# Performance work log

Measured on AMD Instinct MI355X. Metric: run time of the kernel, lower is better.

Reference implementation:

```python
import jax, jax.numpy as jnp
import numpy as np

# PointPillars PillarFeatureNet defaults
VX, VY, VZ = 0.2, 0.2, 4.0
X_OFF = VX / 2 + 0.0
Y_OFF = VY / 2 + (-40.0)
Z_OFF = VZ / 2 + (-3.0)
BN_EPS = 1e-3
N, M, C_RAW, C_IN, C_OUT = 100000, 32, 4, 10, 64


def setup_inputs() -> dict:
    key = jax.random.key(0)
    k1, k2, k3, k4, k5, k6 = jax.random.split(key, 6)
    features = jax.random.normal(k1, (N, M, C_RAW), dtype=jnp.float32)
    num_points = jax.random.randint(k2, (N,), 1, M + 1, dtype=jnp.int32)
    coors = jax.random.randint(k3, (N, 4), 0, 400, dtype=jnp.int32)
    # PFNLayer params: Linear(10 -> 64, bias=False) + BatchNorm1d(64) (eval stats)
    W = jax.random.normal(k4, (C_OUT, C_IN), dtype=jnp.float32) * (1.0 / np.sqrt(C_IN))
    gamma = jnp.ones((C_OUT,), jnp.float32)
    beta = jnp.zeros((C_OUT,), jnp.float32)
    running_mean = jax.random.normal(k5, (C_OUT,), dtype=jnp.float32) * 0.1
    running_var = jnp.abs(jax.random.normal(k6, (C_OUT,), dtype=jnp.float32)) * 0.1 + 0.9
    return {"features": features, "num_points": num_points, "coors": coors,
            "W": W, "gamma": gamma, "beta": beta,
            "running_mean": running_mean, "running_var": running_var}


def reference(features, num_points, coors, W, gamma, beta, running_mean, running_var):
    np_f = num_points.astype(features.dtype)[:, None, None]            # (N,1,1)
    xyz = features[:, :, :3]                                           # (N,M,3)
    # cluster center offset
    points_mean = jnp.sum(xyz, axis=1, keepdims=True) / np_f           # (N,1,3)
    f_cluster = xyz - points_mean                                      # (N,M,3)
    # voxel center offset (coors layout: [batch, z, y, x])
    cz = coors[:, 0].astype(features.dtype)[:, None]
    cy = coors[:, 1].astype(features.dtype)[:, None]
    cx = coors[:, 2].astype(features.dtype)[:, None]
    f_center = jnp.stack([
        features[:, :, 0] - (cx * VX + X_OFF),
        features[:, :, 1] - (cy * VY + Y_OFF),
        features[:, :, 2] - (cz * VZ + Z_OFF),
    ], axis=-1)                                                        # (N,M,3)
    feats = jnp.concatenate([features, f_cluster, f_center], axis=-1)  # (N,M,10)
    # padding mask
    mask = (jnp.arange(M, dtype=jnp.int32)[None, :] < num_points[:, None])
    feats = feats * mask[:, :, None].astype(feats.dtype)
    # PFNLayer: Linear -> BN(eval) -> GELU -> max over points
    x = jnp.einsum('nmc,oc->nmo', feats, W)                            # (N,M,64)
    inv_std = jax.lax.rsqrt(running_var + BN_EPS)
    x = (x - running_mean) * (inv_std * gamma) + beta
    x = jax.nn.gelu(x, approximate=False)
    return jnp.max(x, axis=1)                                          # (N,64)
```

## Files before the change

### kernel.cpp

```cpp
#include <hip/hip_runtime.h>
#include <cmath>


__device__ __forceinline__ float gelu_exact(float x) {
    return 0.5f * x * (1.0f + erff(x * 0.70710678118654752440f));
}

__global__ __launch_bounds__(256) void pfn_kernel(
    const float* __restrict__ features,
    const int*   __restrict__ num_points,
    const int*   __restrict__ coors,
    const float* __restrict__ W,
    const float* __restrict__ gamma,
    const float* __restrict__ beta,
    const float* __restrict__ rmean,
    const float* __restrict__ rvar,
    float*       __restrict__ out,
    int nTotal)
{
    __shared__ float4 lds[4][64];

    const int lane = threadIdx.x & 63;
    const int wid  = threadIdx.x >> 6;
    const int waveGlobal = blockIdx.x * 4 + wid;
    const int waveCount  = gridDim.x * 4;
    const int nPairs = (nTotal + 1) >> 1;

    const int o = lane;
    const float w0 = W[o*10+0], w1 = W[o*10+1], w2 = W[o*10+2], w3 = W[o*10+3],
                w4 = W[o*10+4], w5 = W[o*10+5], w6 = W[o*10+6], w7 = W[o*10+7],
                w8 = W[o*10+8], w9 = W[o*10+9];
    const float a = gamma[o] / sqrtf(rvar[o] + 1e-3f);
    const float b = fmaf(-rmean[o], a, beta[o]);
    const float A0 = a*(w0+w4+w7), A1 = a*(w1+w5+w8), A2 = a*(w2+w6+w9), A3 = a*w3;

    for (int p = waveGlobal; p < nPairs; p += waveCount) {
        const int iA = 2*p;
        const int iB = (2*p + 1 < nTotal) ? (2*p + 1) : (nTotal - 1);
        const bool hasB = (2*p + 1 < nTotal);

        const float4* fb = reinterpret_cast<const float4*>(features) + (size_t)p * 64;
        float4 f = fb[lane];
        lds[wid][lane] = f;

        float sx = f.x, sy = f.y, sz = f.z;
        #pragma unroll
        for (int d = 1; d < 32; d <<= 1) {
            sx += __shfl_xor(sx, d);
            sy += __shfl_xor(sy, d);
            sz += __shfl_xor(sz, d);
        }
        const float tx = __shfl_xor(sx, 32), ty = __shfl_xor(sy, 32), tz = __shfl_xor(sz, 32);
        const bool lo = (lane < 32);
        const float sAx = lo ? sx : tx, sAy = lo ? sy : ty, sAz = lo ? sz : tz;
        const float sBx = lo ? tx : sx, sBy = lo ? ty : sy, sBz = lo ? tz : sz;

        const int nA = num_points[iA];
        const int nB = num_points[iB];
        const int4 cA = reinterpret_cast<const int4*>(coors)[iA];
        const int4 cB = reinterpret_cast<const int4*>(coors)[iB];

        const float mAx = sAx / (float)nA, mAy = sAy / (float)nA, mAz = sAz / (float)nA;
        const float mBx = sBx / (float)nB, mBy = sBy / (float)nB, mBz = sBz / (float)nB;

        const float ccxA = fmaf((float)cA.z, 0.2f,   0.1f);
        const float ccyA = fmaf((float)cA.y, 0.2f, -39.9f);
        const float cczA = fmaf((float)cA.x, 4.0f,  -1.0f);
        const float ccxB = fmaf((float)cB.z, 0.2f,   0.1f);
        const float ccyB = fmaf((float)cB.y, 0.2f, -39.9f);
        const float cczB = fmaf((float)cB.x, 4.0f,  -1.0f);

        const float KA = -(mAx*w4 + mAy*w5 + mAz*w6 + ccxA*w7 + ccyA*w8 + cczA*w9);
        const float KB = -(mBx*w4 + mBy*w5 + mBz*w6 + ccxB*w7 + ccyB*w8 + cczB*w9);
        const float CA = fmaf(a, KA, b);
        const float CB = fmaf(a, KB, b);

        __asm__ volatile("s_waitcnt lgkmcnt(0)" ::: "memory");

        float vmaxA = -INFINITY, vminA = INFINITY;
        const float4* la = &lds[wid][0];
        for (int m = 0; m < nA; ++m) {
            float4 t = la[m];
            float y = fmaf(t.x, A0, fmaf(t.y, A1, fmaf(t.z, A2, fmaf(t.w, A3, CA))));
            vmaxA = fmaxf(vmaxA, y);
            vminA = fminf(vminA, y);
        }
        float vmaxB = -INFINITY, vminB = INFINITY;
        const float4* lb = &lds[wid][32];
        for (int m = 0; m < nB; ++m) {
            float4 t = lb[m];
            float y = fmaf(t.x, A0, fmaf(t.y, A1, fmaf(t.z, A2, fmaf(t.w, A3, CB))));
            vmaxB = fmaxf(vmaxB, y);
            vminB = fminf(vminB, y);
        }
        if (nA < 32) { vmaxA = fmaxf(vmaxA, b); vminA = fminf(vminA, b); }
        if (nB < 32) { vmaxB = fmaxf(vmaxB, b); vminB = fminf(vminB, b); }

        const float rA = fmaxf(gelu_exact(vmaxA), gelu_exact(vminA));
        const float rB = fmaxf(gelu_exact(vmaxB), gelu_exact(vminB));

        out[(size_t)iA * 64 + o] = rA;
        if (hasB) out[(size_t)iB * 64 + o] = rB;
    }
}

extern "C" void kernel_launch(void* const* d_in, const int* in_sizes, int n_in,
                              void* d_out, int out_size, void* d_ws, size_t ws_size,
                              hipStream_t stream) {
    const float* features   = (const float*)d_in[0];
    const int*   num_points = (const int*)  d_in[1];
    const int*   coors      = (const int*)  d_in[2];
    const float* W          = (const float*)d_in[3];
    const float* gamma      = (const float*)d_in[4];
    const float* beta       = (const float*)d_in[5];
    const float* rmean      = (const float*)d_in[6];
    const float* rvar       = (const float*)d_in[7];
    float* out = (float*)d_out;

    const int nTotal = in_sizes[1];

    pfn_kernel<<<2048, 256, 0, stream>>>(features, num_points, coors, W,
                                         gamma, beta, rmean, rvar, out, nTotal);
}
```

Baseline: 135.3 us.

## Transpose pillar points to SoA in LDS and process 8 points per iteration with packed FMA

Stores each pillar's points in structure-of-arrays form in LDS, padding invalid slots with a copy of point 0 so that points can be processed in chunks of 8 without a tail. The inner min/max loop uses v2f packed FMAs with four independent accumulators to raise ILP and allow packed-math issue. Division by the point count is replaced with a hardware reciprocal. The risk is extra shuffles and LDS writes per pair, plus up to 7 wasted points per pillar.

```diff
diff --git a/kernel.cpp b/kernel.cpp
--- a/kernel.cpp
+++ b/kernel.cpp
@@ -2,8 +2,47 @@
 #include <cmath>
 
 
+typedef float v2f __attribute__((ext_vector_type(2)));
+
 __device__ __forceinline__ float gelu_exact(float x) {
     return 0.5f * x * (1.0f + erff(x * 0.70710678118654752440f));
+}
+
+__device__ __forceinline__ void pillar_minmax(const float* __restrict__ R, int n,
+                                              v2f a0, v2f a1, v2f a2, v2f a3, v2f cc,
+                                              float& oMax, float& oMin)
+{
+    float vmx0 = -INFINITY, vmx1 = -INFINITY, vmx2 = -INFINITY, vmx3 = -INFINITY;
+    float vmn0 =  INFINITY, vmn1 =  INFINITY, vmn2 =  INFINITY, vmn3 =  INFINITY;
+    const int t = (n + 7) >> 3;
+    for (int c = 0; c < t; ++c) {
+        const float4* px = (const float4*)(R +   0 + c * 8);
+        const float4* py = (const float4*)(R +  32 + c * 8);
+        const float4* pz = (const float4*)(R +  64 + c * 8);
+        const float4* pw = (const float4*)(R +  96 + c * 8);
+        float4 xa = px[0], xb = px[1];
+        float4 ya = py[0], yb = py[1];
+        float4 za = pz[0], zb = pz[1];
+        float4 wa = pw[0], wb = pw[1];
+        v2f X0 = {xa.x, xa.y}, X1 = {xa.z, xa.w}, X2 = {xb.x, xb.y}, X3 = {xb.z, xb.w};
+        v2f Y0 = {ya.x, ya.y}, Y1 = {ya.z, ya.w}, Y2 = {yb.x, yb.y}, Y3 = {yb.z, yb.w};
+        v2f Z0 = {za.x, za.y}, Z1 = {za.z, za.w}, Z2 = {zb.x, zb.y}, Z3 = {zb.z, zb.w};
+        v2f W0 = {wa.x, wa.y}, W1 = {wa.z, wa.w}, W2 = {wb.x, wb.y}, W3 = {wb.z, wb.w};
+        v2f y0 = __builtin_elementwise_fma(X0, a0, __builtin_elementwise_fma(Y0, a1,
+                 __builtin_elementwise_fma(Z0, a2, __builtin_elementwise_fma(W0, a3, cc))));
+        v2f y1 = __builtin_elementwise_fma(X1, a0, __builtin_elementwise_fma(Y1, a1,
+                 __builtin_elementwise_fma(Z1, a2, __builtin_elementwise_fma(W1, a3, cc))));
+        v2f y2 = __builtin_elementwise_fma(X2, a0, __builtin_elementwise_fma(Y2, a1,
+                 __builtin_elementwise_fma(Z2, a2, __builtin_elementwise_fma(W2, a3, cc))));
+        v2f y3 = __builtin_elementwise_fma(X3, a0, __builtin_elementwise_fma(Y3, a1,
+                 __builtin_elementwise_fma(Z3, a2, __builtin_elementwise_fma(W3, a3, cc))));
+        vmx0 = fmaxf(fmaxf(y0.x, y0.y), vmx0);  vmn0 = fminf(fminf(y0.x, y0.y), vmn0);
+        vmx1 = fmaxf(fmaxf(y1.x, y1.y), vmx1);  vmn1 = fminf(fminf(y1.x, y1.y), vmn1);
+        vmx2 = fmaxf(fmaxf(y2.x, y2.y), vmx2);  vmn2 = fminf(fminf(y2.x, y2.y), vmn2);
+        vmx3 = fmaxf(fmaxf(y3.x, y3.y), vmx3);  vmn3 = fminf(fminf(y3.x, y3.y), vmn3);
+    }
+    oMax = fmaxf(fmaxf(vmx0, vmx1), fmaxf(vmx2, vmx3));
+    oMin = fminf(fminf(vmn0, vmn1), fminf(vmn2, vmn3));
 }
 
 __global__ __launch_bounds__(256) void pfn_kernel(
@@ -18,13 +57,14 @@
     float*       __restrict__ out,
     int nTotal)
 {
-    __shared__ float4 lds[4][64];
+    __shared__ float lds[4][2 * 4 * 32];
 
     const int lane = threadIdx.x & 63;
     const int wid  = threadIdx.x >> 6;
     const int waveGlobal = blockIdx.x * 4 + wid;
     const int waveCount  = gridDim.x * 4;
     const int nPairs = (nTotal + 1) >> 1;
+    float* slot = &lds[wid][0];
 
     const int o = lane;
     const float w0 = W[o*10+0], w1 = W[o*10+1], w2 = W[o*10+2], w3 = W[o*10+3],
@@ -32,16 +72,16 @@
                 w8 = W[o*10+8], w9 = W[o*10+9];
     const float a = gamma[o] / sqrtf(rvar[o] + 1e-3f);
     const float b = fmaf(-rmean[o], a, beta[o]);
-    const float A0 = a*(w0+w4+w7), A1 = a*(w1+w5+w8), A2 = a*(w2+w6+w9), A3 = a*w3;
+    const float A0s = a*(w0+w4+w7), A1s = a*(w1+w5+w8), A2s = a*(w2+w6+w9), A3s = a*w3;
+    const v2f a0 = {A0s, A0s}, a1 = {A1s, A1s}, a2 = {A2s, A2s}, a3 = {A3s, A3s};
 
     for (int p = waveGlobal; p < nPairs; p += waveCount) {
-        const int iA = 2*p;
-        const int iB = (2*p + 1 < nTotal) ? (2*p + 1) : (nTotal - 1);
-        const bool hasB = (2*p + 1 < nTotal);
+        const int iA = 2 * p;
+        const bool hasB = (2 * p + 1 < nTotal);
+        const int iB = hasB ? (2 * p + 1) : (nTotal - 1);
 
         const float4* fb = reinterpret_cast<const float4*>(features) + (size_t)p * 64;
-        float4 f = fb[lane];
-        lds[wid][lane] = f;
+        const float4 f = fb[lane];
 
         float sx = f.x, sy = f.y, sz = f.z;
         #pragma unroll
@@ -51,17 +91,32 @@
             sz += __shfl_xor(sz, d);
         }
         const float tx = __shfl_xor(sx, 32), ty = __shfl_xor(sy, 32), tz = __shfl_xor(sz, 32);
-        const bool lo = (lane < 32);
-        const float sAx = lo ? sx : tx, sAy = lo ? sy : ty, sAz = lo ? sz : tz;
-        const float sBx = lo ? tx : sx, sBy = lo ? ty : sy, sBz = lo ? tz : sz;
 
         const int nA = num_points[iA];
         const int nB = num_points[iB];
         const int4 cA = reinterpret_cast<const int4*>(coors)[iA];
         const int4 cB = reinterpret_cast<const int4*>(coors)[iB];
 
-        const float mAx = sAx / (float)nA, mAy = sAy / (float)nA, mAz = sAz / (float)nA;
-        const float mBx = sBx / (float)nB, mBy = sBy / (float)nB, mBz = sBz / (float)nB;
+        const int m = lane & 31;
+        const int nOwn = (lane < 32) ? nA : nB;
+        const int src = lane & 32;
+        const float f0x = __shfl(f.x, src), f0y = __shfl(f.y, src),
+                    f0z = __shfl(f.z, src), f0w = __shfl(f.w, src);
+        const bool valid = m < nOwn;
+        const int rbase = (lane >> 5) * 128 + m;
+        slot[rbase +  0] = valid ? f.x : f0x;
+        slot[rbase + 32] = valid ? f.y : f0y;
+        slot[rbase + 64] = valid ? f.z : f0z;
+        slot[rbase + 96] = valid ? f.w : f0w;
+
+        const bool lo = (lane < 32);
+        const float sAx = lo ? sx : tx, sAy = lo ? sy : ty, sAz = lo ? sz : tz;
+        const float sBx = lo ? tx : sx, sBy = lo ? ty : sy, sBz = lo ? tz : sz;
+
+        const float rcA = __builtin_amdgcn_rcpf((float)nA);
+        const float rcB = __builtin_amdgcn_rcpf((float)nB);
+        const float mAx = sAx * rcA, mAy = sAy * rcA, mAz = sAz * rcA;
+        const float mBx = sBx * rcB, mBy = sBy * rcB, mBz = sBz * rcB;
 
         const float ccxA = fmaf((float)cA.z, 0.2f,   0.1f);
         const float ccyA = fmaf((float)cA.y, 0.2f, -39.9f);
@@ -77,22 +132,10 @@
 
         __asm__ volatile("s_waitcnt lgkmcnt(0)" ::: "memory");
 
-        float vmaxA = -INFINITY, vminA = INFINITY;
-        const float4* la = &lds[wid][0];
-        for (int m = 0; m < nA; ++m) {
-            float4 t = la[m];
-            float y = fmaf(t.x, A0, fmaf(t.y, A1, fmaf(t.z, A2, fmaf(t.w, A3, CA))));
-            vmaxA = fmaxf(vmaxA, y);
-            vminA = fminf(vminA, y);
-        }
-        float vmaxB = -INFINITY, vminB = INFINITY;
-        const float4* lb = &lds[wid][32];
-        for (int m = 0; m < nB; ++m) {
-            float4 t = lb[m];
-            float y = fmaf(t.x, A0, fmaf(t.y, A1, fmaf(t.z, A2, fmaf(t.w, A3, CB))));
-            vmaxB = fmaxf(vmaxB, y);
-            vminB = fminf(vminB, y);
-        }
+        float vmaxA, vminA, vmaxB, vminB;
+        pillar_minmax(slot,       nA, a0, a1, a2, a3, (v2f){CA, CA}, vmaxA, vminA);
+        pillar_minmax(slot + 128, nB, a0, a1, a2, a3, (v2f){CB, CB}, vmaxB, vminB);
+
         if (nA < 32) { vmaxA = fmaxf(vmaxA, b); vminA = fminf(vminA, b); }
         if (nB < 32) { vmaxB = fmaxf(vmaxB, b); vminB = fminf(vminB, b); }
 
```

New measurement: 137.4 us. No clear change (+1.6%).

## Load pillar points via scalar loads, one pillar per wave, drop LDS

Applied to the files above, without the earlier changes.

Each wave now handles one pillar and pulls its 32 points, num_points and coors straight into scalar registers with inline-asm s_load_dwordx16 in four chunks. The LDS staging and shuffle reduction are gone. The xyz sums are computed from the scalar values, padded slots are replaced by the first point, and C is added after the max/min reduction. This is meant to remove LDS traffic, shuffle latency and the data-dependent loop, but it serializes each chunk behind an lgkmcnt wait and puts all of the feature bandwidth through the scalar cache.

```diff
diff --git a/kernel.cpp b/kernel.cpp
--- a/kernel.cpp
+++ b/kernel.cpp
@@ -2,8 +2,54 @@
 #include <cmath>
 
 
+typedef float v16f __attribute__((ext_vector_type(16)));
+typedef int   v4i  __attribute__((ext_vector_type(4)));
+
 __device__ __forceinline__ float gelu_exact(float x) {
     return 0.5f * x * (1.0f + erff(x * 0.70710678118654752440f));
+}
+
+__device__ __forceinline__ float dotp(float x, float y, float z, float w,
+                                      float A0, float A1, float A2, float A3) {
+    return fmaf(x, A0, fmaf(y, A1, fmaf(z, A2, w * A3)));
+}
+
+struct Acc { float sx, sy, sz, mx, mn; };
+
+__device__ __forceinline__ void proc_chunk(const v16f u0, const v16f u1, int base, int ns,
+                                           float x0, float y0, float z0, float w0,
+                                           float A0, float A1, float A2, float A3, Acc& ac)
+{
+    ac.sx += ((u0[0] + u0[4]) + (u0[8] + u0[12])) + ((u1[0] + u1[4]) + (u1[8] + u1[12]));
+    ac.sy += ((u0[1] + u0[5]) + (u0[9] + u0[13])) + ((u1[1] + u1[5]) + (u1[9] + u1[13]));
+    ac.sz += ((u0[2] + u0[6]) + (u0[10] + u0[14])) + ((u1[2] + u1[6]) + (u1[10] + u1[14]));
+
+    if (ns >= base + 8) {
+        float p0 = dotp(u0[0],  u0[1],  u0[2],  u0[3],  A0, A1, A2, A3);
+        float p1 = dotp(u0[4],  u0[5],  u0[6],  u0[7],  A0, A1, A2, A3);
+        float p2 = dotp(u0[8],  u0[9],  u0[10], u0[11], A0, A1, A2, A3);
+        float p3 = dotp(u0[12], u0[13], u0[14], u0[15], A0, A1, A2, A3);
+        float p4 = dotp(u1[0],  u1[1],  u1[2],  u1[3],  A0, A1, A2, A3);
+        float p5 = dotp(u1[4],  u1[5],  u1[6],  u1[7],  A0, A1, A2, A3);
+        float p6 = dotp(u1[8],  u1[9],  u1[10], u1[11], A0, A1, A2, A3);
+        float p7 = dotp(u1[12], u1[13], u1[14], u1[15], A0, A1, A2, A3);
+        ac.mx = fmaxf(fmaxf(p6, p7), fmaxf(fmaxf(p4, p5),
+                fmaxf(fmaxf(p2, p3), fmaxf(fmaxf(p0, p1), ac.mx))));
+        ac.mn = fminf(fminf(p6, p7), fminf(fminf(p4, p5),
+                fminf(fminf(p2, p3), fminf(fminf(p0, p1), ac.mn))));
+    } else if (ns > base) {
+        #define DOTSEL(u, j)                                                     \
+            { bool vld = (base + (j)) < ns;                                      \
+              float xs_ = vld ? u[4*(j)+0] : x0;                                 \
+              float ys_ = vld ? u[4*(j)+1] : y0;                                 \
+              float zs_ = vld ? u[4*(j)+2] : z0;                                 \
+              float ws_ = vld ? u[4*(j)+3] : w0;                                 \
+              float pv  = dotp(xs_, ys_, zs_, ws_, A0, A1, A2, A3);              \
+              ac.mx = fmaxf(ac.mx, pv); ac.mn = fminf(ac.mn, pv); }
+        DOTSEL(u0, 0) DOTSEL(u0, 1) DOTSEL(u0, 2) DOTSEL(u0, 3)
+        DOTSEL(u1, 0) DOTSEL(u1, 1) DOTSEL(u1, 2) DOTSEL(u1, 3)
+        #undef DOTSEL
+    }
 }
 
 __global__ __launch_bounds__(256) void pfn_kernel(
@@ -18,15 +64,11 @@
     float*       __restrict__ out,
     int nTotal)
 {
-    __shared__ float4 lds[4][64];
-
-    const int lane = threadIdx.x & 63;
-    const int wid  = threadIdx.x >> 6;
+    const int wid = __builtin_amdgcn_readfirstlane(threadIdx.x) >> 6;
     const int waveGlobal = blockIdx.x * 4 + wid;
     const int waveCount  = gridDim.x * 4;
-    const int nPairs = (nTotal + 1) >> 1;
 
-    const int o = lane;
+    const int o = threadIdx.x & 63;
     const float w0 = W[o*10+0], w1 = W[o*10+1], w2 = W[o*10+2], w3 = W[o*10+3],
                 w4 = W[o*10+4], w5 = W[o*10+5], w6 = W[o*10+6], w7 = W[o*10+7],
                 w8 = W[o*10+8], w9 = W[o*10+9];
@@ -34,73 +76,59 @@
     const float b = fmaf(-rmean[o], a, beta[o]);
     const float A0 = a*(w0+w4+w7), A1 = a*(w1+w5+w8), A2 = a*(w2+w6+w9), A3 = a*w3;
 
-    for (int p = waveGlobal; p < nPairs; p += waveCount) {
-        const int iA = 2*p;
-        const int iB = (2*p + 1 < nTotal) ? (2*p + 1) : (nTotal - 1);
-        const bool hasB = (2*p + 1 < nTotal);
+    for (int i = waveGlobal; i < nTotal; i += waveCount) {
+        const float* fptr = features + (size_t)i * 128;
 
-        const float4* fb = reinterpret_cast<const float4*>(features) + (size_t)p * 64;
-        float4 f = fb[lane];
-        lds[wid][lane] = f;
+        int ns; v4i cr; v16f u0, u1;
+        asm volatile(
+            "s_load_dword %0, %4, 0x0\n\t"
+            "s_load_dwordx4 %1, %5, 0x0\n\t"
+            "s_load_dwordx16 %2, %6, 0x0\n\t"
+            "s_load_dwordx16 %3, %6, 0x40\n\t"
+            "s_waitcnt lgkmcnt(0)"
+            : "=&s"(ns), "=&s"(cr), "=&s"(u0), "=&s"(u1)
+            : "s"(num_points + i), "s"(coors + (size_t)4 * i), "s"(fptr));
 
-        float sx = f.x, sy = f.y, sz = f.z;
-        #pragma unroll
-        for (int d = 1; d < 32; d <<= 1) {
-            sx += __shfl_xor(sx, d);
-            sy += __shfl_xor(sy, d);
-            sz += __shfl_xor(sz, d);
-        }
-        const float tx = __shfl_xor(sx, 32), ty = __shfl_xor(sy, 32), tz = __shfl_xor(sz, 32);
-        const bool lo = (lane < 32);
-        const float sAx = lo ? sx : tx, sAy = lo ? sy : ty, sAz = lo ? sz : tz;
-        const float sBx = lo ? tx : sx, sBy = lo ? ty : sy, sBz = lo ? tz : sz;
+        const float x0 = u0[0], y0 = u0[1], z0 = u0[2], w0p = u0[3];
+        Acc ac = { 0.f, 0.f, 0.f, -INFINITY, INFINITY };
 
-        const int nA = num_points[iA];
-        const int nB = num_points[iB];
-        const int4 cA = reinterpret_cast<const int4*>(coors)[iA];
-        const int4 cB = reinterpret_cast<const int4*>(coors)[iB];
+        proc_chunk(u0, u1, 0, ns, x0, y0, z0, w0p, A0, A1, A2, A3, ac);
 
-        const float mAx = sAx / (float)nA, mAy = sAy / (float)nA, mAz = sAz / (float)nA;
-        const float mBx = sBx / (float)nB, mBy = sBy / (float)nB, mBz = sBz / (float)nB;
+        asm volatile(
+            "s_load_dwordx16 %0, %2, 0x80\n\t"
+            "s_load_dwordx16 %1, %2, 0xC0\n\t"
+            "s_waitcnt lgkmcnt(0)"
+            : "=&s"(u0), "=&s"(u1) : "s"(fptr));
+        proc_chunk(u0, u1, 8, ns, x0, y0, z0, w0p, A0, A1, A2, A3, ac);
 
-        const float ccxA = fmaf((float)cA.z, 0.2f,   0.1f);
-        const float ccyA = fmaf((float)cA.y, 0.2f, -39.9f);
-        const float cczA = fmaf((float)cA.x, 4.0f,  -1.0f);
-        const float ccxB = fmaf((float)cB.z, 0.2f,   0.1f);
-        const float ccyB = fmaf((float)cB.y, 0.2f, -39.9f);
-        const float cczB = fmaf((float)cB.x, 4.0f,  -1.0f);
+        asm volatile(
+            "s_load_dwordx16 %0, %2, 0x100\n\t"
+            "s_load_dwordx16 %1, %2, 0x140\n\t"
+            "s_waitcnt lgkmcnt(0)"
+            : "=&s"(u0), "=&s"(u1) : "s"(fptr));
+        proc_chunk(u0, u1, 16, ns, x0, y0, z0, w0p, A0, A1, A2, A3, ac);
 
-        const float KA = -(mAx*w4 + mAy*w5 + mAz*w6 + ccxA*w7 + ccyA*w8 + cczA*w9);
-        const float KB = -(mBx*w4 + mBy*w5 + mBz*w6 + ccxB*w7 + ccyB*w8 + cczB*w9);
-        const float CA = fmaf(a, KA, b);
-        const float CB = fmaf(a, KB, b);
+        asm volatile(
+            "s_load_dwordx16 %0, %2, 0x180\n\t"
+            "s_load_dwordx16 %1, %2, 0x1C0\n\t"
+            "s_waitcnt lgkmcnt(0)"
+            : "=&s"(u0), "=&s"(u1) : "s"(fptr));
+        proc_chunk(u0, u1, 24, ns, x0, y0, z0, w0p, A0, A1, A2, A3, ac);
 
-        __asm__ volatile("s_waitcnt lgkmcnt(0)" ::: "memory");
+        const float rc = __builtin_amdgcn_rcpf((float)ns);
+        const float mx_ = ac.sx * rc, my_ = ac.sy * rc, mz_ = ac.sz * rc;
+        const float ccx = fmaf((float)cr[2], 0.2f,   0.1f);
+        const float ccy = fmaf((float)cr[1], 0.2f, -39.9f);
+        const float ccz = fmaf((float)cr[0], 4.0f,  -1.0f);
+        const float K = -fmaf(mx_, w4, fmaf(my_, w5, fmaf(mz_, w6,
+                         fmaf(ccx, w7, fmaf(ccy, w8, ccz * w9)))));
+        const float C = fmaf(a, K, b);
 
-        float vmaxA = -INFINITY, vminA = INFINITY;
-        const float4* la = &lds[wid][0];
-        for (int m = 0; m < nA; ++m) {
-            float4 t = la[m];
-            float y = fmaf(t.x, A0, fmaf(t.y, A1, fmaf(t.z, A2, fmaf(t.w, A3, CA))));
-            vmaxA = fmaxf(vmaxA, y);
-            vminA = fminf(vminA, y);
-        }
-        float vmaxB = -INFINITY, vminB = INFINITY;
-        const float4* lb = &lds[wid][32];
-        for (int m = 0; m < nB; ++m) {
-            float4 t = lb[m];
-            float y = fmaf(t.x, A0, fmaf(t.y, A1, fmaf(t.z, A2, fmaf(t.w, A3, CB))));
-            vmaxB = fmaxf(vmaxB, y);
-            vminB = fminf(vminB, y);
-        }
-        if (nA < 32) { vmaxA = fmaxf(vmaxA, b); vminA = fminf(vminA, b); }
-        if (nB < 32) { vmaxB = fmaxf(vmaxB, b); vminB = fminf(vminB, b); }
+        float ymax = ac.mx + C, ymin = ac.mn + C;
+        if (ns < 32) { ymax = fmaxf(ymax, b); ymin = fminf(ymin, b); }
 
-        const float rA = fmaxf(gelu_exact(vmaxA), gelu_exact(vminA));
-        const float rB = fmaxf(gelu_exact(vmaxB), gelu_exact(vminB));
-
-        out[(size_t)iA * 64 + o] = rA;
-        if (hasB) out[(size_t)iB * 64 + o] = rB;
+        const float r = fmaxf(gelu_exact(ymax), gelu_exact(ymin));
+        out[(size_t)i * 64 + o] = r;
     }
 }
 
```

After: 184.4 us. +36.4%, slower.
